# Performance work log

Hardware: AMD Instinct MI355X
Metric: run time of the kernel (lower is better)

## Reference

```python
import jax, jax.numpy as jnp
import numpy as np

B, S = 4, 2048          # batch, seq_len
IN, OUT = 4096, 4096    # in_features, out_features
SPARSITY = 0.05         # ortho_ratio: fraction of outlier residual entries
ALPHA = 1.0             # privacy switch (set_privacy) -> residual enabled


def setup_inputs() -> dict:
    key = jax.random.key(0)
    k1, k2, k3, k4, k5 = jax.random.split(key, 5)
    x = jax.random.normal(k1, (B, S, IN), dtype=jnp.float32)
    # packed int4 weights: two (value+8) nibbles per byte, values in [0,15]
    base_packed = jax.random.randint(k2, (OUT, IN // 2), 0, 256, dtype=jnp.int32)
    # per-output-row scales = row_max/7, realistic small magnitudes
    scales = jax.random.uniform(k3, (OUT, 1), dtype=jnp.float32, minval=1e-3, maxval=2e-2)
    mask = jax.random.bernoulli(k4, SPARSITY, (OUT, IN))
    w_ortho = jax.random.normal(k5, (OUT, IN), dtype=jnp.float32) * 0.01 * mask
    return {"x": x, "base_packed": base_packed, "scales": scales, "w_ortho": w_ortho}


def _dequant(base_packed, scales):
    # unpack: even input columns are the low nibble, odd columns the high nibble
    low = base_packed & 0xF
    high = (base_packed >> 4) & 0xF
    offs = jnp.stack([low, high], axis=-1).reshape(base_packed.shape[0], -1)  # [OUT, IN]
    return (offs.astype(jnp.float32) - 8.0) * scales  # int4 value * per-row scale


def reference(x, base_packed, scales, w_ortho):
    # out = x @ (W_base + alpha * W_ortho)^T  (fused dequant-GEMM + CSR residual in the kernel)
    w = _dequant(base_packed, scales) + ALPHA * w_ortho  # [OUT, IN]
    return jnp.einsum('bsi,oi->bso', x, w)  # [B, S, OUT], fp32 like the kernel
```

## Files before the change

### kernel.cpp

```cpp
#include <hip/hip_runtime.h>
#include <stdint.h>


#define M_TOTAL 8192
#define N_TOTAL 4096
#define K_TOTAL 4096

typedef __attribute__((ext_vector_type(8)))  __bf16          bf16x8;
typedef __attribute__((ext_vector_type(4)))  float           floatx4;
typedef __attribute__((ext_vector_type(8)))  unsigned short  ushort8;
typedef __attribute__((ext_vector_type(4)))  float           f32x4;
typedef __attribute__((ext_vector_type(4)))  int             intx4;

__device__ __forceinline__ unsigned short f2bf(float f) {
    union { float f; uint32_t u; } c; c.f = f;
    uint32_t u = c.u + 0x7FFFu + ((c.u >> 16) & 1u);
    return (unsigned short)(u >> 16);
}

#define CVT_BLOCKS 16384
#define DEQ_BLOCKS 8192

__global__ __launch_bounds__(256) void prep_kernel(
    const float* __restrict__ x,
    const int*   __restrict__ packed,
    const float* __restrict__ scales,
    const float* __restrict__ ortho,
    unsigned short* __restrict__ xb,
    unsigned short* __restrict__ wb)
{
    const int blk = blockIdx.x;
    if (blk < CVT_BLOCKS) {
        const size_t t = (size_t)blk * 256 + threadIdx.x;
        const f32x4* xv = (const f32x4*)x;
        f32x4 v0 = xv[2 * t];
        f32x4 v1 = xv[2 * t + 1];
        ushort8 r;
        r[0] = f2bf(v0[0]); r[1] = f2bf(v0[1]); r[2] = f2bf(v0[2]); r[3] = f2bf(v0[3]);
        r[4] = f2bf(v1[0]); r[5] = f2bf(v1[1]); r[6] = f2bf(v1[2]); r[7] = f2bf(v1[3]);
        ((ushort8*)xb)[t] = r;
    } else {
        const int t  = (blk - CVT_BLOCKS) * 256 + threadIdx.x;
        const int o  = t >> 9;
        const int jp = (t & 511) << 2;
        intx4 p = *(const intx4*)(packed + (size_t)o * (K_TOTAL / 2) + jp);
        const float s = scales[o];
        const size_t base = (size_t)o * K_TOTAL + (size_t)jp * 2;
        f32x4 g0 = *(const f32x4*)(ortho + base);
        f32x4 g1 = *(const f32x4*)(ortho + base + 4);
        float g[8] = { g0[0], g0[1], g0[2], g0[3], g1[0], g1[1], g1[2], g1[3] };
        ushort8 r;
#pragma unroll
        for (int i = 0; i < 4; ++i) {
            int pi = p[i];
            float lo = (float)((pi & 0xF) - 8) * s + g[2 * i];
            float hi = (float)(((pi >> 4) & 0xF) - 8) * s + g[2 * i + 1];
            r[2 * i]     = f2bf(lo);
            r[2 * i + 1] = f2bf(hi);
        }
        *(ushort8*)(wb + base) = r;
    }
}

__device__ __forceinline__ void async16(const void* g, void* l) {
    __builtin_amdgcn_global_load_lds(
        (__attribute__((address_space(1))) void*)(g),
        (__attribute__((address_space(3))) void*)(l),
        16, 0, 0);
}

__global__ __launch_bounds__(256) void gemm_bt_kernel(
    const unsigned short* __restrict__ A,
    const unsigned short* __restrict__ Bm,
    float* __restrict__ C)
{
    __shared__ __attribute__((aligned(16))) unsigned short As[2 * 128 * 32];
    __shared__ __attribute__((aligned(16))) unsigned short Bs[2 * 128 * 32];

    const int tid  = threadIdx.x;
    const int wave = tid >> 6;
    const int lane = tid & 63;
    const int quad = lane >> 4;
    const int r16  = lane & 15;

    const int row0 = blockIdx.y * 128;
    const int col0 = blockIdx.x * 128;
    const int m_off = (wave >> 1) * 64;
    const int n_off = (wave & 1) * 64;

    const int sr = tid >> 2;
    const int ct = (tid & 3) ^ ((tid >> 3) & 3);
    const int sc = ct * 8;

    const unsigned short* Ag0 = A  + (size_t)(row0 + sr)      * K_TOTAL + sc;
    const unsigned short* Ag1 = A  + (size_t)(row0 + 64 + sr) * K_TOTAL + sc;
    const unsigned short* Bg0 = Bm + (size_t)(col0 + sr)      * K_TOTAL + sc;
    const unsigned short* Bg1 = Bm + (size_t)(col0 + 64 + sr) * K_TOTAL + sc;

    unsigned short* AsW = As + wave * 512;
    unsigned short* BsW = Bs + wave * 512;

    const int swz   = (r16 >> 1) & 3;
    const int a_ofs = (m_off + r16) * 32 + (quad ^ swz) * 8;
    const int b_ofs = (n_off + r16) * 32 + (quad ^ swz) * 8;

    floatx4 acc[4][4] = {};

    for (int kt = 0; kt < K_TOTAL; kt += 64) {
        __syncthreads();
        async16(Ag0 + kt,      AsW);
        async16(Ag1 + kt,      AsW + 2048);
        async16(Bg0 + kt,      BsW);
        async16(Bg1 + kt,      BsW + 2048);
        async16(Ag0 + kt + 32, AsW + 4096);
        async16(Ag1 + kt + 32, AsW + 4096 + 2048);
        async16(Bg0 + kt + 32, BsW + 4096);
        async16(Bg1 + kt + 32, BsW + 4096 + 2048);
        __syncthreads();

#pragma unroll
        for (int h = 0; h < 2; ++h) {
            bf16x8 a[4], b[4];
#pragma unroll
            for (int i = 0; i < 4; ++i)
                a[i] = *(const bf16x8*)(As + h * 4096 + a_ofs + i * (16 * 32));
#pragma unroll
            for (int i = 0; i < 4; ++i)
                b[i] = *(const bf16x8*)(Bs + h * 4096 + b_ofs + i * (16 * 32));

#pragma unroll
            for (int mi = 0; mi < 4; ++mi)
#pragma unroll
                for (int ni = 0; ni < 4; ++ni)
                    acc[mi][ni] = __builtin_amdgcn_mfma_f32_16x16x32_bf16(
                        a[mi], b[ni], acc[mi][ni], 0, 0, 0);
        }
    }

#pragma unroll
    for (int mi = 0; mi < 4; ++mi) {
#pragma unroll
        for (int ni = 0; ni < 4; ++ni) {
            const int r = row0 + m_off + mi * 16 + quad * 4;
            const int c = col0 + n_off + ni * 16 + r16;
#pragma unroll
            for (int i = 0; i < 4; ++i)
                C[(size_t)(r + i) * N_TOTAL + c] = acc[mi][ni][i];
        }
    }
}

extern "C" void kernel_launch(void* const* d_in, const int* in_sizes, int n_in,
                              void* d_out, int out_size, void* d_ws, size_t ws_size,
                              hipStream_t stream) {
    const float* x      = (const float*)d_in[0];
    const int*   packed = (const int*)d_in[1];
    const float* scales = (const float*)d_in[2];
    const float* ortho  = (const float*)d_in[3];
    float*       out    = (float*)d_out;

    unsigned short* Xb = (unsigned short*)d_ws;
    unsigned short* Wb = (unsigned short*)((char*)d_ws + (size_t)M_TOTAL * K_TOTAL * 2);

    prep_kernel<<<CVT_BLOCKS + DEQ_BLOCKS, 256, 0, stream>>>(x, packed, scales, ortho, Xb, Wb);

    dim3 grid(N_TOTAL / 128, M_TOTAL / 128);
    gemm_bt_kernel<<<grid, 256, 0, stream>>>(Xb, Wb, out);
}
```

Before: 635.6 us.

## Use 256x256 tiles with 512 threads and a 4-stage async LDS pipeline

Replaces the 128x128, 256-thread GEMM with a 256x256 tile computed by 8 waves. Global-to-LDS loads run through a 4-slot ring buffer with explicit vmcnt waits and barriers, so loads for later K slices overlap MFMA work on the current one. The change also raises MFMA priority with s_setprio. Larger tiles increase data reuse and cut global traffic, but the kernel now uses 128 KB of LDS and 128 accumulator registers per lane, and the grid shrinks to 512 blocks.

```diff
diff --git a/kernel.cpp b/kernel.cpp
--- a/kernel.cpp
+++ b/kernel.cpp
@@ -69,80 +69,119 @@
         16, 0, 0);
 }
 
-__global__ __launch_bounds__(256) void gemm_bt_kernel(
+__global__ __launch_bounds__(512, 2) void gemm256_kernel(
     const unsigned short* __restrict__ A,
     const unsigned short* __restrict__ Bm,
     float* __restrict__ C)
 {
-    __shared__ __attribute__((aligned(16))) unsigned short As[2 * 128 * 32];
-    __shared__ __attribute__((aligned(16))) unsigned short Bs[2 * 128 * 32];
+    __shared__ __attribute__((aligned(16))) unsigned short As[4 * 8192];
+    __shared__ __attribute__((aligned(16))) unsigned short Bs[4 * 8192];
 
     const int tid  = threadIdx.x;
     const int wave = tid >> 6;
     const int lane = tid & 63;
     const int quad = lane >> 4;
     const int r16  = lane & 15;
-
-    const int row0 = blockIdx.y * 128;
-    const int col0 = blockIdx.x * 128;
-    const int m_off = (wave >> 1) * 64;
-    const int n_off = (wave & 1) * 64;
+    const int wm   = wave >> 2;
+    const int wn   = wave & 3;
+
+    const int row0 = blockIdx.y * 256;
+    const int col0 = blockIdx.x * 256;
 
     const int sr = tid >> 2;
-    const int ct = (tid & 3) ^ ((tid >> 3) & 3);
-    const int sc = ct * 8;
-
-    const unsigned short* Ag0 = A  + (size_t)(row0 + sr)      * K_TOTAL + sc;
-    const unsigned short* Ag1 = A  + (size_t)(row0 + 64 + sr) * K_TOTAL + sc;
-    const unsigned short* Bg0 = Bm + (size_t)(col0 + sr)      * K_TOTAL + sc;
-    const unsigned short* Bg1 = Bm + (size_t)(col0 + 64 + sr) * K_TOTAL + sc;
+    const int cs = (tid & 3) ^ ((tid >> 3) & 3);
+    const unsigned short* ag0 = A  + (size_t)(row0 + sr) * K_TOTAL + cs * 8;
+    const unsigned short* ag1 = ag0 + (size_t)128 * K_TOTAL;
+    const unsigned short* bg0 = Bm + (size_t)(col0 + sr) * K_TOTAL + cs * 8;
+    const unsigned short* bg1 = bg0 + (size_t)128 * K_TOTAL;
 
     unsigned short* AsW = As + wave * 512;
     unsigned short* BsW = Bs + wave * 512;
 
+#define STAGE_A(slot, kk) do { \
+    async16(ag0 + (kk), AsW + (slot) * 8192); \
+    async16(ag1 + (kk), AsW + (slot) * 8192 + 4096); } while (0)
+#define STAGE_B(slot, kk) do { \
+    async16(bg0 + (kk), BsW + (slot) * 8192); \
+    async16(bg1 + (kk), BsW + (slot) * 8192 + 4096); } while (0)
+
     const int swz   = (r16 >> 1) & 3;
-    const int a_ofs = (m_off + r16) * 32 + (quad ^ swz) * 8;
-    const int b_ofs = (n_off + r16) * 32 + (quad ^ swz) * 8;
-
-    floatx4 acc[4][4] = {};
-
-    for (int kt = 0; kt < K_TOTAL; kt += 64) {
-        __syncthreads();
-        async16(Ag0 + kt,      AsW);
-        async16(Ag1 + kt,      AsW + 2048);
-        async16(Bg0 + kt,      BsW);
-        async16(Bg1 + kt,      BsW + 2048);
-        async16(Ag0 + kt + 32, AsW + 4096);
-        async16(Ag1 + kt + 32, AsW + 4096 + 2048);
-        async16(Bg0 + kt + 32, BsW + 4096);
-        async16(Bg1 + kt + 32, BsW + 4096 + 2048);
-        __syncthreads();
-
-#pragma unroll
-        for (int h = 0; h < 2; ++h) {
-            bf16x8 a[4], b[4];
-#pragma unroll
-            for (int i = 0; i < 4; ++i)
-                a[i] = *(const bf16x8*)(As + h * 4096 + a_ofs + i * (16 * 32));
-#pragma unroll
-            for (int i = 0; i < 4; ++i)
-                b[i] = *(const bf16x8*)(Bs + h * 4096 + b_ofs + i * (16 * 32));
-
-#pragma unroll
-            for (int mi = 0; mi < 4; ++mi)
-#pragma unroll
-                for (int ni = 0; ni < 4; ++ni)
-                    acc[mi][ni] = __builtin_amdgcn_mfma_f32_16x16x32_bf16(
-                        a[mi], b[ni], acc[mi][ni], 0, 0, 0);
-        }
+    const int a_ofs = (wm * 128 + r16) * 32 + ((quad ^ swz) << 3);
+    const int b_ofs = (wn * 64  + r16) * 32 + ((quad ^ swz) << 3);
+
+#define LDA(slot, m) (*(const bf16x8*)(As + (slot) * 8192 + a_ofs + (m) * 512))
+#define LDB(slot, n) (*(const bf16x8*)(Bs + (slot) * 8192 + b_ofs + (n) * 512))
+
+    floatx4 acc[8][4] = {};
+
+#define MROW(mi, ar) \
+    acc[mi][0] = __builtin_amdgcn_mfma_f32_16x16x32_bf16(ar, b0, acc[mi][0], 0, 0, 0); \
+    acc[mi][1] = __builtin_amdgcn_mfma_f32_16x16x32_bf16(ar, b1, acc[mi][1], 0, 0, 0); \
+    acc[mi][2] = __builtin_amdgcn_mfma_f32_16x16x32_bf16(ar, b2, acc[mi][2], 0, 0, 0); \
+    acc[mi][3] = __builtin_amdgcn_mfma_f32_16x16x32_bf16(ar, b3, acc[mi][3], 0, 0, 0);
+
+#define SLICE(slot, DOSTAGE, kkst, VMW) do { \
+    bf16x8 b0 = LDB(slot, 0), b1 = LDB(slot, 1), b2 = LDB(slot, 2), b3 = LDB(slot, 3); \
+    bf16x8 a0 = LDA(slot, 0), a1 = LDA(slot, 1), a2 = LDA(slot, 2), a3 = LDA(slot, 3); \
+    if (DOSTAGE) STAGE_A(((slot) + 3) & 3, kkst); \
+    __builtin_amdgcn_s_barrier(); \
+    asm volatile("s_waitcnt lgkmcnt(0)"); \
+    __builtin_amdgcn_s_setprio(1); \
+    MROW(0, a0) MROW(1, a1) MROW(2, a2) MROW(3, a3) \
+    __builtin_amdgcn_s_setprio(0); \
+    __builtin_amdgcn_s_barrier(); \
+    bf16x8 a4 = LDA(slot, 4), a5 = LDA(slot, 5), a6 = LDA(slot, 6), a7 = LDA(slot, 7); \
+    if (DOSTAGE) STAGE_B(((slot) + 3) & 3, kkst); \
+    __builtin_amdgcn_s_barrier(); \
+    asm volatile("s_waitcnt lgkmcnt(0)"); \
+    __builtin_amdgcn_s_setprio(1); \
+    MROW(4, a4) MROW(5, a5) MROW(6, a6) MROW(7, a7) \
+    __builtin_amdgcn_s_setprio(0); \
+    asm volatile(VMW); \
+    __builtin_amdgcn_s_barrier(); \
+} while (0)
+
+    STAGE_A(0, 0);  STAGE_B(0, 0);
+    STAGE_A(1, 32); STAGE_B(1, 32);
+    STAGE_A(2, 64); STAGE_B(2, 64);
+    STAGE_A(3, 96); STAGE_B(3, 96);
+    asm volatile("s_waitcnt vmcnt(12)");
+    __builtin_amdgcn_s_barrier();
+
+    SLICE(0, 0, 0,      "s_waitcnt vmcnt(8)");
+    SLICE(1, 1, 4 * 32, "s_waitcnt vmcnt(8)");
+    SLICE(2, 1, 5 * 32, "s_waitcnt vmcnt(8)");
+    SLICE(3, 1, 6 * 32, "s_waitcnt vmcnt(8)");
+
+#pragma unroll 1
+    for (int s4 = 4; s4 <= 120; s4 += 4) {
+        const int kkb = (s4 + 3) * 32;
+        SLICE(0, 1, kkb,      "s_waitcnt vmcnt(8)");
+        SLICE(1, 1, kkb + 32, "s_waitcnt vmcnt(8)");
+        SLICE(2, 1, kkb + 64, "s_waitcnt vmcnt(8)");
+        SLICE(3, 1, kkb + 96, "s_waitcnt vmcnt(8)");
     }
 
-#pragma unroll
-    for (int mi = 0; mi < 4; ++mi) {
+    SLICE(0, 1, 127 * 32, "s_waitcnt vmcnt(8)");
+    SLICE(1, 0, 0,        "s_waitcnt vmcnt(4)");
+    SLICE(2, 0, 0,        "s_waitcnt vmcnt(0)");
+    SLICE(3, 0, 0,        "");
+
+#undef SLICE
+#undef MROW
+#undef LDA
+#undef LDB
+#undef STAGE_A
+#undef STAGE_B
+
+    const int r_base = row0 + wm * 128 + quad * 4;
+    const int c_base = col0 + wn * 64 + r16;
+#pragma unroll
+    for (int mi = 0; mi < 8; ++mi) {
 #pragma unroll
         for (int ni = 0; ni < 4; ++ni) {
-            const int r = row0 + m_off + mi * 16 + quad * 4;
-            const int c = col0 + n_off + ni * 16 + r16;
+            const int r = r_base + mi * 16;
+            const int c = c_base + ni * 16;
 #pragma unroll
             for (int i = 0; i < 4; ++i)
                 C[(size_t)(r + i) * N_TOTAL + c] = acc[mi][ni][i];
@@ -164,6 +203,6 @@
 
     prep_kernel<<<CVT_BLOCKS + DEQ_BLOCKS, 256, 0, stream>>>(x, packed, scales, ortho, Xb, Wb);
 
-    dim3 grid(N_TOTAL / 128, M_TOTAL / 128);
-    gemm_bt_kernel<<<grid, 256, 0, stream>>>(Xb, Wb, out);
-}
+    dim3 grid(N_TOTAL / 256, M_TOTAL / 256);
+    gemm256_kernel<<<grid, 512, 0, stream>>>(Xb, Wb, out);
+}
```

Result: faster. 532.4 us (-16.2%).

## Replace GEMM with 256x256 tile, 8-wave software-pipelined kernel using barriers and setprio

Applied to the files above, without the earlier changes.

Rewrites the bf16 GEMM to use 256x256 block tiles with 512 threads (8 waves), each wave owning a 64x32-per-quadrant subtile. Loads for the next K-tile are issued into LDS in four staggered quarters interleaved with MFMA clusters, using explicit vmcnt/lgkmcnt waits, raw barriers, sched_barrier and setprio to overlap global loads, LDS reads and matrix math. B fragments are double-buffered in registers across tiles and the LDS layout uses an XOR swizzle over 64-element rows. This targets the old kernel's lack of overlap (loads and compute serialized by two syncthreads per tile) and its lower arithmetic intensity, at the cost of higher register pressure and a fragile hand-scheduled pipeline.

```diff
diff --git a/kernel.cpp b/kernel.cpp
--- a/kernel.cpp
+++ b/kernel.cpp
@@ -69,80 +69,156 @@
         16, 0, 0);
 }
 
-__global__ __launch_bounds__(256) void gemm_bt_kernel(
+__global__ __launch_bounds__(512, 2) void gemm256_kernel(
     const unsigned short* __restrict__ A,
     const unsigned short* __restrict__ Bm,
     float* __restrict__ C)
 {
-    __shared__ __attribute__((aligned(16))) unsigned short As[2 * 128 * 32];
-    __shared__ __attribute__((aligned(16))) unsigned short Bs[2 * 128 * 32];
+    __shared__ __attribute__((aligned(16))) unsigned short As[16384];
+    __shared__ __attribute__((aligned(16))) unsigned short Bs[16384];
 
     const int tid  = threadIdx.x;
     const int wave = tid >> 6;
     const int lane = tid & 63;
     const int quad = lane >> 4;
     const int r16  = lane & 15;
-
-    const int row0 = blockIdx.y * 128;
-    const int col0 = blockIdx.x * 128;
-    const int m_off = (wave >> 1) * 64;
-    const int n_off = (wave & 1) * 64;
-
-    const int sr = tid >> 2;
-    const int ct = (tid & 3) ^ ((tid >> 3) & 3);
-    const int sc = ct * 8;
-
-    const unsigned short* Ag0 = A  + (size_t)(row0 + sr)      * K_TOTAL + sc;
-    const unsigned short* Ag1 = A  + (size_t)(row0 + 64 + sr) * K_TOTAL + sc;
-    const unsigned short* Bg0 = Bm + (size_t)(col0 + sr)      * K_TOTAL + sc;
-    const unsigned short* Bg1 = Bm + (size_t)(col0 + 64 + sr) * K_TOTAL + sc;
-
-    unsigned short* AsW = As + wave * 512;
-    unsigned short* BsW = Bs + wave * 512;
-
-    const int swz   = (r16 >> 1) & 3;
-    const int a_ofs = (m_off + r16) * 32 + (quad ^ swz) * 8;
-    const int b_ofs = (n_off + r16) * 32 + (quad ^ swz) * 8;
-
-    floatx4 acc[4][4] = {};
-
-    for (int kt = 0; kt < K_TOTAL; kt += 64) {
-        __syncthreads();
-        async16(Ag0 + kt,      AsW);
-        async16(Ag1 + kt,      AsW + 2048);
-        async16(Bg0 + kt,      BsW);
-        async16(Bg1 + kt,      BsW + 2048);
-        async16(Ag0 + kt + 32, AsW + 4096);
-        async16(Ag1 + kt + 32, AsW + 4096 + 2048);
-        async16(Bg0 + kt + 32, BsW + 4096);
-        async16(Bg1 + kt + 32, BsW + 4096 + 2048);
-        __syncthreads();
-
-#pragma unroll
-        for (int h = 0; h < 2; ++h) {
-            bf16x8 a[4], b[4];
-#pragma unroll
-            for (int i = 0; i < 4; ++i)
-                a[i] = *(const bf16x8*)(As + h * 4096 + a_ofs + i * (16 * 32));
-#pragma unroll
-            for (int i = 0; i < 4; ++i)
-                b[i] = *(const bf16x8*)(Bs + h * 4096 + b_ofs + i * (16 * 32));
-
-#pragma unroll
-            for (int mi = 0; mi < 4; ++mi)
-#pragma unroll
-                for (int ni = 0; ni < 4; ++ni)
-                    acc[mi][ni] = __builtin_amdgcn_mfma_f32_16x16x32_bf16(
-                        a[mi], b[ni], acc[mi][ni], 0, 0, 0);
-        }
+    const int s8   = r16 & 7;
+    const int wm   = wave >> 2;
+    const int wn   = wave & 3;
+
+    const int row0 = blockIdx.y * 256;
+    const int col0 = blockIdx.x * 256;
+
+    const int w16l  = wave * 16 + (lane >> 3);
+    const int c_src = (lane & 7) ^ ((lane >> 3) & 7);
+    const unsigned short* agA0 = A  + (size_t)(row0 + w16l) * K_TOTAL + c_src * 8;
+    const unsigned short* agA1 = agA0 + (size_t)128 * K_TOTAL;
+    const unsigned short* bgB0 = Bm + (size_t)(col0 + w16l) * K_TOTAL + c_src * 8;
+    const unsigned short* bgB1 = bgB0 + (size_t)128 * K_TOTAL;
+    unsigned short* dA0 = As + wave * 1024;
+    unsigned short* dA1 = As + 8192 + wave * 1024;
+    unsigned short* dB0 = Bs + wave * 1024;
+    unsigned short* dB1 = Bs + 8192 + wave * 1024;
+
+#define STG(dst, src, T) do { \
+    async16((src) + (size_t)(T) * 64, (dst)); \
+    async16((src) + (size_t)(T) * 64 + (size_t)8 * K_TOTAL, (dst) + 512); } while (0)
+
+    const int ck0 = ((0 + quad) ^ s8) * 8;
+    const int ck1 = ((4 + quad) ^ s8) * 8;
+#define AROW(mi) ((((mi) < 4 ? wm * 64 + (mi) * 16 : 128 + wm * 64 + ((mi) - 4) * 16) + r16) * 64)
+#define BROW(ni) ((((ni) < 2 ? wn * 32 + (ni) * 16 : 128 + wn * 32 + ((ni) - 2) * 16) + r16) * 64)
+#define LDSA(mi, ckk) (*(const bf16x8*)(As + AROW(mi) + (ckk)))
+#define LDSB(ni, ckk) (*(const bf16x8*)(Bs + BROW(ni) + (ckk)))
+
+    floatx4 acc[8][4] = {};
+
+#define MM(mi, ni, af, bf) \
+    acc[mi][ni] = __builtin_amdgcn_mfma_f32_16x16x32_bf16(af, bf, acc[mi][ni], 0, 0, 0);
+#define C8(m0, aA, aB, aC, aD, n0, bX, bY) \
+    MM(m0 + 0, n0, aA, bX) MM(m0 + 0, n0 + 1, aA, bY) \
+    MM(m0 + 1, n0, aB, bX) MM(m0 + 1, n0 + 1, aB, bY) \
+    MM(m0 + 2, n0, aC, bX) MM(m0 + 2, n0 + 1, aC, bY) \
+    MM(m0 + 3, n0, aD, bX) MM(m0 + 3, n0 + 1, aD, bY)
+
+#define BAR    __builtin_amdgcn_s_barrier()
+#define LGKM0  asm volatile("s_waitcnt lgkmcnt(0)")
+#define VM4    asm volatile("s_waitcnt vmcnt(4)")
+#define PRIO1  __builtin_amdgcn_s_setprio(1)
+#define PRIO0  __builtin_amdgcn_s_setprio(0)
+#define SCHED0 __builtin_amdgcn_sched_barrier(0)
+
+    bf16x8 bbAk0_0, bbAk0_1, bbAk1_0, bbAk1_1;
+    bf16x8 bbBk0_0, bbBk0_1, bbBk1_0, bbBk1_1;
+
+#define TILE(T, CUR, NXT, DOSTG) do { \
+     \
+    bf16x8 a0k0_0 = LDSA(0, ck0), a0k0_1 = LDSA(1, ck0), a0k0_2 = LDSA(2, ck0), a0k0_3 = LDSA(3, ck0); \
+    bf16x8 a0k1_0 = LDSA(0, ck1), a0k1_1 = LDSA(1, ck1), a0k1_2 = LDSA(2, ck1), a0k1_3 = LDSA(3, ck1); \
+    if (DOSTG) STG(dB0, bgB0, (T) + 1); \
+    VM4; BAR; LGKM0; PRIO1; \
+    C8(0, a0k0_0, a0k0_1, a0k0_2, a0k0_3, 0, bb##CUR##k0_0, bb##CUR##k0_1) \
+    C8(0, a0k1_0, a0k1_1, a0k1_2, a0k1_3, 0, bb##CUR##k1_0, bb##CUR##k1_1) \
+    PRIO0; BAR; SCHED0; \
+     \
+    bf16x8 b1k0_2 = LDSB(2, ck0), b1k0_3 = LDSB(3, ck0); \
+    bf16x8 b1k1_2 = LDSB(2, ck1), b1k1_3 = LDSB(3, ck1); \
+    if (DOSTG) STG(dA0, agA0, (T) + 1); \
+    VM4; BAR; LGKM0; PRIO1; \
+    C8(0, a0k0_0, a0k0_1, a0k0_2, a0k0_3, 2, b1k0_2, b1k0_3) \
+    C8(0, a0k1_0, a0k1_1, a0k1_2, a0k1_3, 2, b1k1_2, b1k1_3) \
+    PRIO0; BAR; SCHED0; \
+     \
+    bf16x8 a1k0_0 = LDSA(4, ck0), a1k0_1 = LDSA(5, ck0), a1k0_2 = LDSA(6, ck0), a1k0_3 = LDSA(7, ck0); \
+    bf16x8 a1k1_0 = LDSA(4, ck1), a1k1_1 = LDSA(5, ck1), a1k1_2 = LDSA(6, ck1), a1k1_3 = LDSA(7, ck1); \
+    if (DOSTG) STG(dB1, bgB1, (T) + 1); \
+    VM4; BAR; LGKM0; PRIO1; \
+    C8(4, a1k0_0, a1k0_1, a1k0_2, a1k0_3, 2, b1k0_2, b1k0_3) \
+    C8(4, a1k1_0, a1k1_1, a1k1_2, a1k1_3, 2, b1k1_2, b1k1_3) \
+    PRIO0; BAR; SCHED0; \
+     \
+    bb##NXT##k0_0 = LDSB(0, ck0); bb##NXT##k0_1 = LDSB(1, ck0); \
+    bb##NXT##k1_0 = LDSB(0, ck1); bb##NXT##k1_1 = LDSB(1, ck1); \
+    if (DOSTG) STG(dA1, agA1, (T) + 1); \
+    VM4; BAR; LGKM0; PRIO1; \
+    C8(4, a1k0_0, a1k0_1, a1k0_2, a1k0_3, 0, bb##CUR##k0_0, bb##CUR##k0_1) \
+    C8(4, a1k1_0, a1k1_1, a1k1_2, a1k1_3, 0, bb##CUR##k1_0, bb##CUR##k1_1) \
+    PRIO0; BAR; SCHED0; \
+} while (0)
+
+#define TAIL(CUR) do { \
+    bf16x8 a0k0_0 = LDSA(0, ck0), a0k0_1 = LDSA(1, ck0), a0k0_2 = LDSA(2, ck0), a0k0_3 = LDSA(3, ck0); \
+    bf16x8 a0k1_0 = LDSA(0, ck1), a0k1_1 = LDSA(1, ck1), a0k1_2 = LDSA(2, ck1), a0k1_3 = LDSA(3, ck1); \
+    asm volatile("s_waitcnt vmcnt(2)"); BAR; LGKM0; PRIO1; \
+    C8(0, a0k0_0, a0k0_1, a0k0_2, a0k0_3, 0, bb##CUR##k0_0, bb##CUR##k0_1) \
+    C8(0, a0k1_0, a0k1_1, a0k1_2, a0k1_3, 0, bb##CUR##k1_0, bb##CUR##k1_1) \
+    PRIO0; BAR; SCHED0; \
+    bf16x8 b1k0_2 = LDSB(2, ck0), b1k0_3 = LDSB(3, ck0); \
+    bf16x8 b1k1_2 = LDSB(2, ck1), b1k1_3 = LDSB(3, ck1); \
+    asm volatile("s_waitcnt vmcnt(0)"); BAR; LGKM0; PRIO1; \
+    C8(0, a0k0_0, a0k0_1, a0k0_2, a0k0_3, 2, b1k0_2, b1k0_3) \
+    C8(0, a0k1_0, a0k1_1, a0k1_2, a0k1_3, 2, b1k1_2, b1k1_3) \
+    PRIO0; BAR; SCHED0; \
+    bf16x8 a1k0_0 = LDSA(4, ck0), a1k0_1 = LDSA(5, ck0), a1k0_2 = LDSA(6, ck0), a1k0_3 = LDSA(7, ck0); \
+    bf16x8 a1k1_0 = LDSA(4, ck1), a1k1_1 = LDSA(5, ck1), a1k1_2 = LDSA(6, ck1), a1k1_3 = LDSA(7, ck1); \
+    BAR; LGKM0; PRIO1; \
+    C8(4, a1k0_0, a1k0_1, a1k0_2, a1k0_3, 2, b1k0_2, b1k0_3) \
+    C8(4, a1k1_0, a1k1_1, a1k1_2, a1k1_3, 2, b1k1_2, b1k1_3) \
+    C8(4, a1k0_0, a1k0_1, a1k0_2, a1k0_3, 0, bb##CUR##k0_0, bb##CUR##k0_1) \
+    C8(4, a1k1_0, a1k1_1, a1k1_2, a1k1_3, 0, bb##CUR##k1_0, bb##CUR##k1_1) \
+    PRIO0; \
+} while (0)
+
+    STG(dB0, bgB0, 0); STG(dA0, agA0, 0); STG(dB1, bgB1, 0); STG(dA1, agA1, 0);
+    asm volatile("s_waitcnt vmcnt(0)");
+    BAR; SCHED0;
+    bbAk0_0 = LDSB(0, ck0); bbAk0_1 = LDSB(1, ck0);
+    bbAk1_0 = LDSB(0, ck1); bbAk1_1 = LDSB(1, ck1);
+
+#pragma unroll 1
+    for (int T = 0; T < 62; T += 2) {
+        TILE(T,     A, B, 1);
+        TILE(T + 1, B, A, 1);
     }
-
-#pragma unroll
-    for (int mi = 0; mi < 4; ++mi) {
+    TILE(62, A, B, 1);
+    TAIL(B);
+
+#undef TILE
+#undef TAIL
+#undef C8
+#undef MM
+#undef LDSA
+#undef LDSB
+#undef AROW
+#undef BROW
+#undef STG
+
+#pragma unroll
+    for (int mi = 0; mi < 8; ++mi) {
+        const int r = row0 + (mi < 4 ? wm * 64 + mi * 16 : 128 + wm * 64 + (mi - 4) * 16) + quad * 4;
 #pragma unroll
         for (int ni = 0; ni < 4; ++ni) {
-            const int r = row0 + m_off + mi * 16 + quad * 4;
-            const int c = col0 + n_off + ni * 16 + r16;
+            const int c = col0 + (ni < 2 ? wn * 32 + ni * 16 : 128 + wn * 32 + (ni - 2) * 16) + r16;
 #pragma unroll
             for (int i = 0; i < 4; ++i)
                 C[(size_t)(r + i) * N_TOTAL + c] = acc[mi][ni][i];
@@ -164,6 +240,6 @@
 
     prep_kernel<<<CVT_BLOCKS + DEQ_BLOCKS, 256, 0, stream>>>(x, packed, scales, ortho, Xb, Wb);
 
-    dim3 grid(N_TOTAL / 128, M_TOTAL / 128);
-    gemm_bt_kernel<<<grid, 256, 0, stream>>>(Xb, Wb, out);
-}
+    dim3 grid(N_TOTAL / 256, M_TOTAL / 256);
+    gemm256_kernel<<<grid, 512, 0, stream>>>(Xb, Wb, out);
+}
```

Result: no change. 626.0 us (-1.5%).
